# Kernel tuning notes

Hardware: AMD Instinct MI355X
Metric: run time of the kernel (lower is better)

## Reference

```python
import jax, jax.numpy as jnp
import numpy as np

DIAG_PENALTY = 100.0

def setup_inputs() -> dict:
    key = jax.random.key(0)
    x = jax.random.normal(key, (8192, 768), dtype=jnp.float32)
    return {"x": x, "coef": 1.0, "tau": 1.0}

def _similarity(x):
    # sim[i, j] = -||x_i - x_j||^2, computed via GEMM expansion
    # ||a - b||^2 = ||a||^2 + ||b||^2 - 2 a.b  (avoids the (N,N,D) intermediate)
    sq = jnp.sum(x * x, axis=1)                      # [N]
    gram = x @ x.T                                   # [N, N]
    sim = 2.0 * gram - sq[:, None] - sq[None, :]     # = -||x_i - x_j||^2
    n = x.shape[0]
    sim = sim - DIAG_PENALTY * jnp.eye(n, dtype=x.dtype)
    return sim

def reference(x, coef, tau):
    sim = _similarity(x) * tau                       # [N, N]
    logp = jax.nn.log_softmax(sim, axis=-1)          # stable, single pass
    prob = jnp.exp(logp)
    entropy = -jnp.sum(prob * logp, axis=-1)         # [N]
    return coef * jnp.mean(entropy)
```

## Files before the change

kernel.cpp:

```cpp
#include <hip/hip_runtime.h>
#include <hip/hip_bf16.h>
#include <hip/hip_fp8.h>
#include <cstdint>
#include <cstddef>

#define GN 8192
#define GD 768
#define NB 64
#define NTILE 2080
#define KI 12

#define LOG2E 1.4426950408889634f
#define LN2 0.6931471805599453f

typedef __attribute__((ext_vector_type(4))) float f32x4;
typedef __attribute__((ext_vector_type(16))) float f32x16;
typedef __attribute__((ext_vector_type(4))) int i32x4;
typedef __attribute__((ext_vector_type(8))) int i32x8;

typedef __attribute__((address_space(1))) const unsigned int gu32;
typedef __attribute__((address_space(3))) unsigned int lu32;

#define SHUF8(L, H) __builtin_shufflevector(L, H, 0, 1, 2, 3, 4, 5, 6, 7)
#define Z16 {0.f, 0.f, 0.f, 0.f, 0.f, 0.f, 0.f, 0.f, 0.f, 0.f, 0.f, 0.f, 0.f, 0.f, 0.f, 0.f}
#define MXFMA(A, B, C) __builtin_amdgcn_mfma_scale_f32_32x32x64_f8f6f4( \
    A, B, C, 0, 0, 0, 0x7f7f7f7f, 0, 0x7f7f7f7f)

__device__ __forceinline__ void gl2lds16(const void* g, void* l) {
    __builtin_amdgcn_global_load_lds((gu32*)g, (lu32*)l, 16, 0, 0);
}

__device__ __forceinline__ float hexp2(float x) {
    return __builtin_amdgcn_exp2f(x);
}

template <int CTRL>
__device__ __forceinline__ float fdpp(float x) {
    return __int_as_float(__builtin_amdgcn_update_dpp(
        0, __float_as_int(x), CTRL, 0xF, 0xF, true));
}
__device__ __forceinline__ float qmax16(float v) {
    v = fmaxf(v, fdpp<0x128>(v));
    v = fmaxf(v, fdpp<0x124>(v));
    v = fmaxf(v, fdpp<0x122>(v));
    v = fmaxf(v, fdpp<0x121>(v));
    return v;
}
__device__ __forceinline__ float qsum16(float v) {
    v += fdpp<0x128>(v);
    v += fdpp<0x124>(v);
    v += fdpp<0x122>(v);
    v += fdpp<0x121>(v);
    return v;
}

__global__ __launch_bounds__(256) void prep_kernel(const float* __restrict__ x,
                                                   unsigned char* __restrict__ xq,
                                                   float* __restrict__ sq,
                                                   float* __restrict__ out) {
    if (blockIdx.x == 0 && threadIdx.x == 0) out[0] = 0.f;
    const int w = threadIdx.x >> 6, lane = threadIdx.x & 63;
    const int row = blockIdx.x * 4 + w;
    const float4* xr = (const float4*)(x + (size_t)row * GD);
    unsigned int* xqr = (unsigned int*)(xq + (size_t)row * GD);
    float s = 0.f;
#pragma unroll
    for (int i = 0; i < 3; ++i) {
        float4 v = xr[lane + 64 * i];
        unsigned int pk = __builtin_amdgcn_cvt_pk_fp8_f32(v.x, v.y, 0, false);
        pk = __builtin_amdgcn_cvt_pk_fp8_f32(v.z, v.w, pk, true);
        float d0 = __builtin_amdgcn_cvt_f32_fp8(pk, 0);
        float d1 = __builtin_amdgcn_cvt_f32_fp8(pk, 1);
        float d2 = __builtin_amdgcn_cvt_f32_fp8(pk, 2);
        float d3 = __builtin_amdgcn_cvt_f32_fp8(pk, 3);
        s += d0 * d0 + d1 * d1 + d2 * d2 + d3 * d3;
        xqr[lane + 64 * i] = pk;
    }
#pragma unroll
    for (int off = 1; off < 64; off <<= 1) s += __shfl_xor(s, off);
    if (lane == 0) sq[row] = s;
}

__global__ __launch_bounds__(256, 3) void sym_gemm_entropy(
    const unsigned char* __restrict__ xq, const float* __restrict__ sq,
    const float* __restrict__ taup, float* __restrict__ pm,
    float* __restrict__ ps, float* __restrict__ pt) {
    __shared__ __align__(16) char lds[49152];
    float (*tmrg)[4][3] = (float (*)[4][3])lds;

    const int tid = threadIdx.x;
    const int lane = tid & 63;
    const int w = tid >> 6;
    const int cl2 = lane & 31, hi = lane >> 5;

    const int b = blockIdx.x;
    int I = (int)((sqrtf(8.0f * (float)b + 1.0f) - 1.0f) * 0.5f);
    while ((I + 1) * (I + 2) / 2 <= b) ++I;
    while (I * (I + 1) / 2 > b) --I;
    const int J = b - I * (I + 1) / 2;
    const int row_base = I * 128;
    const int col_base = J * 128;
    const float taub = (*taup) * LOG2E;

    const int sS = tid & 127;
    const int g0S = tid >> 7;
    const int qloS = (sS >> 6) & 1, qhiS = (sS >> 5) & 1;
    const int r4S = (sS >> 4) & 1, r3S = (sS >> 3) & 1;
    const int rlowS = (sS & 7) ^ ((qhiS << 1) | r4S);
    const int rS = (r4S << 4) | (r3S << 3) | rlowS;
    const int qS = (qhiS << 1) | qloS;
    const unsigned char* gA = xq + (size_t)(row_base + g0S * 32 + rS) * GD + qS * 16;
    const unsigned char* gB = xq + (size_t)(col_base + g0S * 32 + rS) * GD + qS * 16;

    const int r4L = (cl2 >> 4) & 1, r3L = (cl2 >> 3) & 1;
    const int bsl = (cl2 & 7) ^ ((hi << 1) | r4L);
    const int s0 = (hi << 5) | (r4L << 4) | (r3L << 3) | bsl;
    const int offA0 = w * 2048 + (s0 << 4), offA1 = offA0 + 1024;
    const int offB00 = 8192 + 0 * 2048 + (s0 << 4), offB01 = offB00 + 1024;
    const int offB10 = 8192 + 1 * 2048 + (s0 << 4), offB11 = offB10 + 1024;
    const int offB20 = 8192 + 2 * 2048 + (s0 << 4), offB21 = offB20 + 1024;
    const int offB30 = 8192 + 3 * 2048 + (s0 << 4), offB31 = offB30 + 1024;

    f32x16 acc0 = Z16, acc1 = Z16, acc2 = Z16, acc3 = Z16;

#define STAGE(BUF, KO)                                                \
    do {                                                              \
        char* bn_ = lds + (BUF) * 16384;                              \
        gl2lds16(gA + (KO), bn_ + tid * 16);                          \
        gl2lds16(gA + (size_t)64 * GD + (KO), bn_ + 4096 + tid * 16); \
        gl2lds16(gB + (KO), bn_ + 8192 + tid * 16);                   \
        gl2lds16(gB + (size_t)64 * GD + (KO), bn_ + 12288 + tid * 16);\
    } while (0)

    STAGE(0, 0);
    STAGE(1, 64);

#pragma unroll
    for (int kk = 0; kk < KI; ++kk) {
        if (kk < KI - 1)
            asm volatile("s_waitcnt vmcnt(4)" ::: "memory");
        else
            asm volatile("s_waitcnt vmcnt(0)" ::: "memory");
        __builtin_amdgcn_s_barrier();
        asm volatile("" ::: "memory");

        const char* Ab = lds + (kk % 3) * 16384;
        i32x4 aL = *(const i32x4*)(Ab + offA0), aH = *(const i32x4*)(Ab + offA1);
        i32x4 b0L = *(const i32x4*)(Ab + offB00), b0H = *(const i32x4*)(Ab + offB01);
        i32x4 b1L = *(const i32x4*)(Ab + offB10), b1H = *(const i32x4*)(Ab + offB11);
        i32x4 b2L = *(const i32x4*)(Ab + offB20), b2H = *(const i32x4*)(Ab + offB21);
        i32x4 b3L = *(const i32x4*)(Ab + offB30), b3H = *(const i32x4*)(Ab + offB31);

        if (kk + 2 < KI) STAGE((kk + 2) % 3, (kk + 2) * 64);

        i32x8 av = SHUF8(aL, aH);
        acc0 = MXFMA(av, SHUF8(b0L, b0H), acc0);
        acc1 = MXFMA(av, SHUF8(b1L, b1H), acc1);
        acc2 = MXFMA(av, SHUF8(b2L, b2H), acc2);
        acc3 = MXFMA(av, SHUF8(b3L, b3H), acc3);
    }
#undef STAGE

    f32x4 pa[4][4];
#define SPLIT16(TJ, A)                                          \
    pa[TJ][0] = __builtin_shufflevector(A, A, 0, 1, 2, 3);      \
    pa[TJ][1] = __builtin_shufflevector(A, A, 4, 5, 6, 7);      \
    pa[TJ][2] = __builtin_shufflevector(A, A, 8, 9, 10, 11);    \
    pa[TJ][3] = __builtin_shufflevector(A, A, 12, 13, 14, 15);
    SPLIT16(0, acc0)
    SPLIT16(1, acc1)
    SPLIT16(2, acc2)
    SPLIT16(3, acc3)
#undef SPLIT16

    const float t2 = 2.f * taub;
    const float pen = 100.f * taub;
    float ar[16];
#pragma unroll
    for (int q = 0; q < 4; ++q)
#pragma unroll
        for (int rg = 0; rg < 4; ++rg)
            ar[q * 4 + rg] = -taub * sq[row_base + w * 32 + rg + 8 * q + 4 * hi];
    float ac[4];
#pragma unroll
    for (int tj = 0; tj < 4; ++tj) ac[tj] = -taub * sq[col_base + tj * 32 + cl2];

    float* pmJ = pm + (size_t)J * GN;
    float* psJ = ps + (size_t)J * GN;
    float* ptJ = pt + (size_t)J * GN;

#pragma unroll
    for (int q = 0; q < 4; ++q)
#pragma unroll
        for (int rg = 0; rg < 4; ++rg) {
            const int rl = rg + 8 * q + 4 * hi;
            const int rglob = row_base + w * 32 + rl;
            float uu[4];
            float mloc = -1e30f;
            if (I == J) {
#pragma unroll
                for (int tj = 0; tj < 4; ++tj) {
                    float u = fmaf(t2, pa[tj][q][rg], ac[tj]);
                    if (rglob == col_base + tj * 32 + cl2) u -= pen;
                    uu[tj] = u;
                    mloc = fmaxf(mloc, u);
                }
            } else {
#pragma unroll
                for (int tj = 0; tj < 4; ++tj) {
                    float u = fmaf(t2, pa[tj][q][rg], ac[tj]);
                    uu[tj] = u;
                    mloc = fmaxf(mloc, u);
                }
            }
            mloc = fmaxf(mloc, __shfl_xor(mloc, 16));
            mloc = qmax16(mloc);
            float s = 0.f, t = 0.f;
#pragma unroll
            for (int tj = 0; tj < 4; ++tj) {
                float d = uu[tj] - mloc;
                float e = hexp2(d);
                s += e;
                t += e * d;
            }
            s += __shfl_xor(s, 16);
            t += __shfl_xor(t, 16);
            s = qsum16(s);
            t = qsum16(t);
            if (cl2 == 0) {
                pmJ[rglob] = mloc + ar[q * 4 + rg];
                psJ[rglob] = s;
                ptJ[rglob] = t;
            }
        }

    if (I != J) {
        __syncthreads();
#pragma unroll
        for (int tj = 0; tj < 4; ++tj) {
            float uu[16];
            float mloc = -1e30f;
#pragma unroll
            for (int q = 0; q < 4; ++q)
#pragma unroll
                for (int rg = 0; rg < 4; ++rg) {
                    float u = fmaf(t2, pa[tj][q][rg], ar[q * 4 + rg]);
                    uu[q * 4 + rg] = u;
                    mloc = fmaxf(mloc, u);
                }
            mloc = fmaxf(mloc, __shfl_xor(mloc, 32));
            float s = 0.f, t = 0.f;
#pragma unroll
            for (int k = 0; k < 16; ++k) {
                float d = uu[k] - mloc;
                float e = hexp2(d);
                s += e;
                t += e * d;
            }
            s += __shfl_xor(s, 32);
            t += __shfl_xor(t, 32);
            if (hi == 0) {
                int c = tj * 32 + cl2;
                tmrg[c][w][0] = mloc + ac[tj];
                tmrg[c][w][1] = s;
                tmrg[c][w][2] = t;
            }
        }
        __syncthreads();
        if (tid < 128) {
            float m = tmrg[tid][0][0], S = tmrg[tid][0][1], T = tmrg[tid][0][2];
#pragma unroll
            for (int ww = 1; ww < 4; ++ww) {
                float mc = tmrg[tid][ww][0], Sc = tmrg[tid][ww][1], Tc = tmrg[tid][ww][2];
                float mn = fmaxf(m, mc);
                float ea = hexp2(m - mn), eb = hexp2(mc - mn);
                T = (T + (m - mn) * S) * ea + (Tc + (mc - mn) * Sc) * eb;
                S = S * ea + Sc * eb;
                m = mn;
            }
            int c = col_base + tid;
            pm[(size_t)I * GN + c] = m;
            ps[(size_t)I * GN + c] = S;
            pt[(size_t)I * GN + c] = T;
        }
    }
}

__global__ __launch_bounds__(256) void combine(const float* __restrict__ pm,
                                               const float* __restrict__ ps,
                                               const float* __restrict__ pt,
                                               const float* __restrict__ coefp,
                                               float* __restrict__ out) {
    const int t = threadIdx.x;
    const int r = t & 63;
    const int chunk = t >> 6;
    const int row = blockIdx.x * 64 + r;
    float m = -1e30f, S = 0.f, T = 0.f;
#pragma unroll
    for (int i = 0; i < 16; ++i) {
        const int c = chunk * 16 + i;
        float mc = pm[(size_t)c * GN + row];
        float Sc = ps[(size_t)c * GN + row];
        float Tc = pt[(size_t)c * GN + row];
        float mn = fmaxf(m, mc);
        float ea = __builtin_amdgcn_exp2f(m - mn), eb = __builtin_amdgcn_exp2f(mc - mn);
        T = (T + (m - mn) * S) * ea + (Tc + (mc - mn) * Sc) * eb;
        S = S * ea + Sc * eb;
        m = mn;
    }
    __shared__ float lm[4][64], lS[4][64], lT[4][64];
    lm[chunk][r] = m;
    lS[chunk][r] = S;
    lT[chunk][r] = T;
    __syncthreads();
    if (t < 64) {
        float M = lm[0][r], Sa = lS[0][r], Ta = lT[0][r];
#pragma unroll
        for (int cc = 1; cc < 4; ++cc) {
            float mc = lm[cc][r], Sc = lS[cc][r], Tc = lT[cc][r];
            float mn = fmaxf(M, mc);
            float ea = __builtin_amdgcn_exp2f(M - mn), eb = __builtin_amdgcn_exp2f(mc - mn);
            Ta = (Ta + (M - mn) * Sa) * ea + (Tc + (mc - mn) * Sc) * eb;
            Sa = Sa * ea + Sc * eb;
            M = mn;
        }
        float ent2 = __log2f(Sa) - Ta / Sa;
#pragma unroll
        for (int off = 1; off < 64; off <<= 1) ent2 += __shfl_xor(ent2, off);
        if (t == 0) atomicAdd(out, ent2 * coefp[0] * (LN2 / (float)GN));
    }
}

extern "C" void kernel_launch(void* const* d_in, const int* in_sizes, int n_in,
                              void* d_out, int out_size, void* d_ws, size_t ws_size,
                              hipStream_t stream) {
    const float* x = (const float*)d_in[0];
    const float* coefp = (const float*)d_in[1];
    const float* taup = (const float*)d_in[2];
    float* out = (float*)d_out;

    char* ws = (char*)d_ws;
    unsigned char* xq = (unsigned char*)ws;
    float* sq = (float*)(ws + 6291456);
    float* pm = (float*)(ws + 6324224);
    float* ps = (float*)(ws + 6324224 + 2097152);
    float* pt = (float*)(ws + 6324224 + 2 * 2097152);

    prep_kernel<<<GN / 4, 256, 0, stream>>>(x, xq, sq, out);
    sym_gemm_entropy<<<NTILE, 256, 0, stream>>>(xq, sq, taup, pm, ps, pt);
    combine<<<GN / 64, 256, 0, stream>>>(pm, ps, pt, coefp, out);
}
```

Baseline: 141.6 us.

## Switch GEMM K-loop to double-buffered 128-wide stages with fewer barriers

The FP8 MFMA main loop moves from triple-buffered 64-wide K stages with explicit vmcnt waits to double-buffered 128-wide stages. Each iteration now loads twice as much data and issues eight MFMAs per barrier, halving the number of barriers and iterations. In exchange, LDS grows to 64 KB and the launch bound drops from 3 to 2 blocks per CU, reducing occupancy. The prefetch distance also shrinks to one stage, and a full __syncthreads replaces the finer-grained vmcnt waits.

```diff
diff --git a/kernel.cpp b/kernel.cpp
--- a/kernel.cpp
+++ b/kernel.cpp
@@ -8,7 +8,7 @@
 #define GD 768
 #define NB 64
 #define NTILE 2080
-#define KI 12
+#define KI2 6
 
 #define LOG2E 1.4426950408889634f
 #define LN2 0.6931471805599453f
@@ -81,11 +81,11 @@
     if (lane == 0) sq[row] = s;
 }
 
-__global__ __launch_bounds__(256, 3) void sym_gemm_entropy(
+__global__ __launch_bounds__(256, 2) void sym_gemm_entropy(
     const unsigned char* __restrict__ xq, const float* __restrict__ sq,
     const float* __restrict__ taup, float* __restrict__ pm,
     float* __restrict__ ps, float* __restrict__ pt) {
-    __shared__ __align__(16) char lds[49152];
+    __shared__ __align__(16) char lds[65536];
     float (*tmrg)[4][3] = (float (*)[4][3])lds;
 
     const int tid = threadIdx.x;
@@ -115,49 +115,59 @@
     const int r4L = (cl2 >> 4) & 1, r3L = (cl2 >> 3) & 1;
     const int bsl = (cl2 & 7) ^ ((hi << 1) | r4L);
     const int s0 = (hi << 5) | (r4L << 4) | (r3L << 3) | bsl;
-    const int offA0 = w * 2048 + (s0 << 4), offA1 = offA0 + 1024;
-    const int offB00 = 8192 + 0 * 2048 + (s0 << 4), offB01 = offB00 + 1024;
-    const int offB10 = 8192 + 1 * 2048 + (s0 << 4), offB11 = offB10 + 1024;
-    const int offB20 = 8192 + 2 * 2048 + (s0 << 4), offB21 = offB20 + 1024;
-    const int offB30 = 8192 + 3 * 2048 + (s0 << 4), offB31 = offB30 + 1024;
+    const int offA00 = 0 * 8192 + w * 2048 + (s0 << 4), offA01 = offA00 + 1024;
+    const int offA10 = 1 * 8192 + w * 2048 + (s0 << 4), offA11 = offA10 + 1024;
+    const int offB000 = 16384 + 0 * 2048 + (s0 << 4), offB001 = offB000 + 1024;
+    const int offB010 = 16384 + 1 * 2048 + (s0 << 4), offB011 = offB010 + 1024;
+    const int offB020 = 16384 + 2 * 2048 + (s0 << 4), offB021 = offB020 + 1024;
+    const int offB030 = 16384 + 3 * 2048 + (s0 << 4), offB031 = offB030 + 1024;
 
     f32x16 acc0 = Z16, acc1 = Z16, acc2 = Z16, acc3 = Z16;
 
-#define STAGE(BUF, KO)                                                \
-    do {                                                              \
-        char* bn_ = lds + (BUF) * 16384;                              \
-        gl2lds16(gA + (KO), bn_ + tid * 16);                          \
-        gl2lds16(gA + (size_t)64 * GD + (KO), bn_ + 4096 + tid * 16); \
-        gl2lds16(gB + (KO), bn_ + 8192 + tid * 16);                   \
-        gl2lds16(gB + (size_t)64 * GD + (KO), bn_ + 12288 + tid * 16);\
+#define STAGE(BUF, KO)                                                      \
+    do {                                                                    \
+        char* bn_ = lds + (BUF) * 32768;                                    \
+        gl2lds16(gA + (KO), bn_ + tid * 16);                                \
+        gl2lds16(gA + (size_t)64 * GD + (KO), bn_ + 4096 + tid * 16);       \
+        gl2lds16(gA + 64 + (KO), bn_ + 8192 + tid * 16);                    \
+        gl2lds16(gA + (size_t)64 * GD + 64 + (KO), bn_ + 12288 + tid * 16); \
+        gl2lds16(gB + (KO), bn_ + 16384 + tid * 16);                        \
+        gl2lds16(gB + (size_t)64 * GD + (KO), bn_ + 20480 + tid * 16);      \
+        gl2lds16(gB + 64 + (KO), bn_ + 24576 + tid * 16);                   \
+        gl2lds16(gB + (size_t)64 * GD + 64 + (KO), bn_ + 28672 + tid * 16); \
     } while (0)
 
     STAGE(0, 0);
-    STAGE(1, 64);
-
-#pragma unroll
-    for (int kk = 0; kk < KI; ++kk) {
-        if (kk < KI - 1)
-            asm volatile("s_waitcnt vmcnt(4)" ::: "memory");
-        else
-            asm volatile("s_waitcnt vmcnt(0)" ::: "memory");
-        __builtin_amdgcn_s_barrier();
-        asm volatile("" ::: "memory");
-
-        const char* Ab = lds + (kk % 3) * 16384;
-        i32x4 aL = *(const i32x4*)(Ab + offA0), aH = *(const i32x4*)(Ab + offA1);
-        i32x4 b0L = *(const i32x4*)(Ab + offB00), b0H = *(const i32x4*)(Ab + offB01);
-        i32x4 b1L = *(const i32x4*)(Ab + offB10), b1H = *(const i32x4*)(Ab + offB11);
-        i32x4 b2L = *(const i32x4*)(Ab + offB20), b2H = *(const i32x4*)(Ab + offB21);
-        i32x4 b3L = *(const i32x4*)(Ab + offB30), b3H = *(const i32x4*)(Ab + offB31);
-
-        if (kk + 2 < KI) STAGE((kk + 2) % 3, (kk + 2) * 64);
-
-        i32x8 av = SHUF8(aL, aH);
-        acc0 = MXFMA(av, SHUF8(b0L, b0H), acc0);
-        acc1 = MXFMA(av, SHUF8(b1L, b1H), acc1);
-        acc2 = MXFMA(av, SHUF8(b2L, b2H), acc2);
-        acc3 = MXFMA(av, SHUF8(b3L, b3H), acc3);
+
+#pragma unroll 2
+    for (int kk = 0; kk < KI2; ++kk) {
+        __syncthreads();
+
+        const char* Ab = lds + (kk & 1) * 32768;
+        i32x4 a0L = *(const i32x4*)(Ab + offA00), a0H = *(const i32x4*)(Ab + offA01);
+        i32x4 b00L = *(const i32x4*)(Ab + offB000), b00H = *(const i32x4*)(Ab + offB001);
+        i32x4 b01L = *(const i32x4*)(Ab + offB010), b01H = *(const i32x4*)(Ab + offB011);
+        i32x4 b02L = *(const i32x4*)(Ab + offB020), b02H = *(const i32x4*)(Ab + offB021);
+        i32x4 b03L = *(const i32x4*)(Ab + offB030), b03H = *(const i32x4*)(Ab + offB031);
+
+        if (kk + 1 < KI2) STAGE((kk + 1) & 1, (kk + 1) * 128);
+
+        i32x8 av0 = SHUF8(a0L, a0H);
+        acc0 = MXFMA(av0, SHUF8(b00L, b00H), acc0);
+        acc1 = MXFMA(av0, SHUF8(b01L, b01H), acc1);
+        acc2 = MXFMA(av0, SHUF8(b02L, b02H), acc2);
+        acc3 = MXFMA(av0, SHUF8(b03L, b03H), acc3);
+
+        i32x4 a1L = *(const i32x4*)(Ab + offA10), a1H = *(const i32x4*)(Ab + offA11);
+        i32x4 b10L = *(const i32x4*)(Ab + 8192 + offB000), b10H = *(const i32x4*)(Ab + 8192 + offB001);
+        i32x4 b11L = *(const i32x4*)(Ab + 8192 + offB010), b11H = *(const i32x4*)(Ab + 8192 + offB011);
+        i32x4 b12L = *(const i32x4*)(Ab + 8192 + offB020), b12H = *(const i32x4*)(Ab + 8192 + offB021);
+        i32x4 b13L = *(const i32x4*)(Ab + 8192 + offB030), b13H = *(const i32x4*)(Ab + 8192 + offB031);
+        i32x8 av1 = SHUF8(a1L, a1H);
+        acc0 = MXFMA(av1, SHUF8(b10L, b10H), acc0);
+        acc1 = MXFMA(av1, SHUF8(b11L, b11H), acc1);
+        acc2 = MXFMA(av1, SHUF8(b12L, b12H), acc2);
+        acc3 = MXFMA(av1, SHUF8(b13L, b13H), acc3);
     }
 #undef STAGE
 
```

New measurement: 157.3 us. 11.1% more time.
